# Kernel optimization log

Hardware: AMD Instinct MI355X
Metric: run time of the kernel (lower is better)

## Reference

```python
import jax, jax.numpy as jnp
import numpy as np

EMBED = 768
HEADS = 12
HEAD_DIM = EMBED // HEADS
RANK = 16
EPS = 1e-6
SCALE = 1.0 / np.sqrt(HEAD_DIM)


def setup_inputs() -> dict:
    key = jax.random.key(0)
    ks = jax.random.split(key, 12)
    B, S = 4, 1024
    hidden_states = jax.random.normal(ks[0], (B, S, EMBED), dtype=jnp.float32)
    attention_mask = jnp.zeros((B, 1, 1, S), dtype=jnp.float32)
    w = lambda k: jax.random.normal(k, (EMBED, EMBED), dtype=jnp.float32) * 0.02
    b = lambda k: jax.random.normal(k, (EMBED,), dtype=jnp.float32) * 0.02
    A = jax.random.normal(ks[9], (HEADS, HEAD_DIM, RANK), dtype=jnp.float32) * 0.05
    return {
        "hidden_states": hidden_states,
        "attention_mask": attention_mask,
        "Wq": w(ks[1]), "bq": b(ks[2]),
        "Wk": w(ks[3]), "bk": b(ks[4]),
        "Wv": w(ks[5]), "bv": b(ks[6]),
        "Wo": w(ks[7]), "bo": b(ks[8]),
        "A": A,
    }


def reference(hidden_states, attention_mask, Wq, bq, Wk, bk, Wv, bv, Wo, bo, A):
    B, S, E = hidden_states.shape
    H, D = HEADS, HEAD_DIM

    def proj(W, bias):
        y = hidden_states @ W.T + bias          # (B,S,E), torch Linear: x W^T + b
        return y.reshape(B, S, H, D).transpose(0, 2, 1, 3)  # (B,H,S,D)

    q = proj(Wq, bq)
    k = proj(Wk, bk)
    v = proj(Wv, bv)

    # Low-rank SPD Mahalanobis: G_h = A_h A_h^T + eps*I
    # d^2(x,y) = ||A^T(x-y)||^2 + eps*||x-y||^2 (block-diagonal per batch)
    qA = jnp.einsum("bhsd,hdr->bhsr", q, A)    # (B,H,S,R)
    kA = jnp.einsum("bhsd,hdr->bhsr", k, A)
    qq = jnp.sum(qA * qA, -1) + EPS * jnp.sum(q * q, -1)  # (B,H,S)
    kk = jnp.sum(kA * kA, -1) + EPS * jnp.sum(k * k, -1)
    cross = jnp.einsum("bhsr,bhtr->bhst", qA, kA) + EPS * jnp.einsum("bhsd,bhtd->bhst", q, k)
    d2 = qq[..., :, None] + kk[..., None, :] - 2.0 * cross  # (B,H,S,S)

    scores = -d2 * SCALE + attention_mask      # mask broadcasts (B,1,1,S)
    weights = jax.nn.softmax(scores, axis=-1)  # dropout p is identity in eval
    ctx = jnp.einsum("bhst,bhtd->bhsd", weights, v)
    ctx = ctx.transpose(0, 2, 1, 3).reshape(B, S, E)
    return ctx @ Wo.T + bo
```

## Files before the change

kernel.cpp:

```cpp
#include <hip/hip_runtime.h>

typedef __attribute__((ext_vector_type(8))) short s16x8;
typedef __attribute__((ext_vector_type(4))) float f32x4;
typedef __attribute__((ext_vector_type(4))) unsigned int u32x4;
typedef unsigned short u16;
typedef unsigned int u32;
typedef unsigned long long u64;

__device__ __forceinline__ u16 f2bf(float f) {
  u32 u = __float_as_uint(f);
  u32 r = u + 0x7fffu + ((u >> 16) & 1u);
  return (u16)(r >> 16);
}
__device__ __forceinline__ float bf2f(u16 h) {
  return __uint_as_float(((u32)h) << 16);
}

typedef __attribute__((address_space(3))) char lds_char_t;
typedef __attribute__((address_space(1))) const char glb_char_t;
__device__ __forceinline__ void gl2lds16(const void* g, void* l) {
  __builtin_amdgcn_global_load_lds((glb_char_t*)g, (lds_char_t*)l, 16, 0, 0);
}

#define HS_N 3145728
#define W_N  589824

__global__ __launch_bounds__(256) void convert_kernel(
    const float* __restrict__ hs, const float* __restrict__ wq, const float* __restrict__ wk,
    const float* __restrict__ wv, const float* __restrict__ wo,
    const float* __restrict__ bq, const float* __restrict__ bk, const float* __restrict__ bv,
    u16* __restrict__ hsb, u16* __restrict__ wqkvb, u16* __restrict__ wob,
    float* __restrict__ biasqkv)
{
  int t = blockIdx.x * 256 + threadIdx.x;
  long i = (long)t * 8;
  const float* src;
  u16* dst;
  if (i < HS_N)              { src = hs + i;                  dst = hsb + i; }
  else if (i < HS_N + W_N)   { src = wq + (i - HS_N);         dst = wqkvb + (i - HS_N); }
  else if (i < HS_N + 2*W_N) { src = wk + (i - HS_N - W_N);   dst = wqkvb + (i - HS_N); }
  else if (i < HS_N + 3*W_N) { src = wv + (i - HS_N - 2*W_N); dst = wqkvb + (i - HS_N); }
  else                       { src = wo + (i - HS_N - 3*W_N); dst = wob + (i - HS_N - 3*W_N); }
  float4 a = ((const float4*)src)[0];
  float4 b = ((const float4*)src)[1];
  uint4 o;
  o.x = (u32)f2bf(a.x) | ((u32)f2bf(a.y) << 16);
  o.y = (u32)f2bf(a.z) | ((u32)f2bf(a.w) << 16);
  o.z = (u32)f2bf(b.x) | ((u32)f2bf(b.y) << 16);
  o.w = (u32)f2bf(b.z) | ((u32)f2bf(b.w) << 16);
  *(uint4*)dst = o;
  if (t < 2304) biasqkv[t] = (t < 768) ? bq[t] : ((t < 1536) ? bk[t - 768] : bv[t - 1536]);
}

template<int MODE>
__global__ __launch_bounds__(256, 2) void gemm_bt(
    const u16* __restrict__ A, const u16* __restrict__ Bt, const float* __restrict__ bias,
    float* __restrict__ outF, u16* __restrict__ Qb, u16* __restrict__ Kb, u16* __restrict__ Vtb)
{
  constexpr int NT = (MODE == 0) ? 18 : 6;
  constexpr int CPX = NT * 64 / 8;

  __shared__ __align__(16) char sm[73728];
  char* const smA = sm;
  char* const smB = sm + 24576;

  const int tid = threadIdx.x;
  const int lane = tid & 63;
  const int w = tid >> 6;
  const int l15 = lane & 15, g = lane >> 4;
  const int wid = (blockIdx.x & 7) * CPX + (blockIdx.x >> 3);
  const int bx = wid % NT, by = wid / NT;
  const int mBase = by * 64;
  const int nBase = bx * 128;
  const int wr = w >> 1, wc = w & 1;
  const int mW = wr * 32, nW = wc * 64;

  f32x4 zero = {0.f, 0.f, 0.f, 0.f};
  f32x4 acc[2][4];
  #pragma unroll
  for (int i = 0; i < 2; i++)
    #pragma unroll
    for (int j = 0; j < 4; j++) acc[i][j] = zero;

  const u16* Arow = A + (long)mBase * 768;
  const u16* Brow = Bt + (long)nBase * 768;

  auto stage = [&](int c, int kb) {
    const int k0 = c * 64;
    #pragma unroll
    for (int i = 0; i < 2; i++) {
      int o = (i * 256 + tid) * 16;
      int r = o >> 7;
      int sl = ((o >> 4) & 7) ^ (r & 7);
      gl2lds16(Arow + (long)r * 768 + k0 + sl * 8,
               smA + kb * 8192 + i * 4096 + w * 1024);
    }
    #pragma unroll
    for (int i = 0; i < 4; i++) {
      int o = (i * 256 + tid) * 16;
      int r = o >> 7;
      int sl = ((o >> 4) & 7) ^ (r & 7);
      gl2lds16(Brow + (long)r * 768 + k0 + sl * 8,
               smB + kb * 16384 + i * 4096 + w * 1024);
    }
  };

  auto compute = [&](int kb) {
    const char* bufA = smA + kb * 8192;
    const char* bufB = smB + kb * 16384;
    #pragma unroll
    for (int kh = 0; kh < 2; kh++) {
      s16x8 af[2], bf[4];
      #pragma unroll
      for (int mi = 0; mi < 2; mi++) {
        int R = mW + mi * 16 + l15;
        af[mi] = *(const s16x8*)(bufA + R * 128 + (((kh * 4 + g) ^ (l15 & 7)) << 4));
      }
      #pragma unroll
      for (int ni = 0; ni < 4; ni++) {
        int R = nW + ni * 16 + l15;
        bf[ni] = *(const s16x8*)(bufB + R * 128 + (((kh * 4 + g) ^ (l15 & 7)) << 4));
      }
      #pragma unroll
      for (int mi = 0; mi < 2; mi++)
        #pragma unroll
        for (int ni = 0; ni < 4; ni++)
          acc[mi][ni] = __builtin_amdgcn_mfma_f32_16x16x32_bf16(af[mi], bf[ni], acc[mi][ni], 0, 0, 0);
    }
  };

  auto body = [&](int c, int kb, int kbn) {
    if (c < 11) { stage(c + 1, kbn); asm volatile("s_waitcnt vmcnt(6)" ::: "memory"); }
    else        { asm volatile("s_waitcnt vmcnt(0)" ::: "memory"); }
    asm volatile("s_barrier" ::: "memory");
    compute(kb);
  };

  stage(0, 0);
  #pragma unroll 1
  for (int cc = 0; cc < 4; cc++) {
    body(cc * 3,     0, 1);
    body(cc * 3 + 1, 1, 2);
    body(cc * 3 + 2, 2, 0);
  }
  __syncthreads();

  const int b_ = mBase >> 10;
  const int s0b = mBase & 1023;

  if constexpr (MODE == 1) {
    #pragma unroll
    for (int mi = 0; mi < 2; mi++)
      #pragma unroll
      for (int ni = 0; ni < 4; ni++) {
        int n = nBase + nW + ni * 16 + l15;
        int m0 = mBase + mW + mi * 16 + g * 4;
        float bb = bias[n];
        outF[(long)m0 * 768 + n]       = acc[mi][ni][0] + bb;
        outF[(long)(m0 + 1) * 768 + n] = acc[mi][ni][1] + bb;
        outF[(long)(m0 + 2) * 768 + n] = acc[mi][ni][2] + bb;
        outF[(long)(m0 + 3) * 768 + n] = acc[mi][ni][3] + bb;
      }
  } else {
    const int typ = bx / 6;
    if (typ < 2) {
      u16* qk = (typ == 0) ? Qb : Kb;
      #pragma unroll
      for (int mi = 0; mi < 2; mi++)
        #pragma unroll
        for (int ni = 0; ni < 4; ni++) {
          int n = nBase + nW + ni * 16 + l15;
          int hn = n - typ * 768;
          int h = hn >> 6, d = hn & 63;
          long bh = (long)b_ * 12 + h;
          int s0 = s0b + mW + mi * 16 + g * 4;
          float bb = bias[n];
          u16* dst = qk + (bh << 16) + ((long)s0 << 6) + d;
          dst[0]   = f2bf(acc[mi][ni][0] + bb);
          dst[64]  = f2bf(acc[mi][ni][1] + bb);
          dst[128] = f2bf(acc[mi][ni][2] + bb);
          dst[192] = f2bf(acc[mi][ni][3] + bb);
        }
    } else {
      u16* ct = (u16*)sm;
      #pragma unroll
      for (int mi = 0; mi < 2; mi++)
        #pragma unroll
        for (int ni = 0; ni < 4; ni++) {
          int nr = nW + ni * 16 + l15;
          int mr = mW + mi * 16 + g * 4;
          float bb = bias[nBase + nr];
          u32 lo = (u32)f2bf(acc[mi][ni][0] + bb) | ((u32)f2bf(acc[mi][ni][1] + bb) << 16);
          u32 hi = (u32)f2bf(acc[mi][ni][2] + bb) | ((u32)f2bf(acc[mi][ni][3] + bb) << 16);
          *(u64*)(ct + nr * 72 + mr) = (u64)lo | ((u64)hi << 32);
        }
      __syncthreads();
      int dr = tid >> 1, part = tid & 1;
      int hn = (bx - 12) * 128 + dr;
      int h = hn >> 6, d = hn & 63;
      long bh = (long)b_ * 12 + h;
      u16* dst = Vtb + (bh << 16) + (d << 10) + s0b + part * 32;
      const u16* srl = ct + dr * 72 + part * 32;
      #pragma unroll
      for (int i = 0; i < 4; i++)
        *(uint4*)(dst + i * 8) = *(const uint4*)(srl + i * 8);
    }
  }
}

__global__ __launch_bounds__(256) void qk_ext_kernel(
    const u16* __restrict__ Qb, const u16* __restrict__ Kb, const float* __restrict__ Am,
    const float* __restrict__ mask, u16* __restrict__ qAe, u16* __restrict__ kAe,
    float* __restrict__ beta2)
{
  const bool isK = blockIdx.x >= 192;
  const int rb = blockIdx.x * 256 - (isK ? 49152 : 0);
  const int h = (rb >> 10) % 12;
  const int row = rb + threadIdx.x;
  const int bh = row >> 10;
  const int s = row & 1023;
  const int b_ = bh / 12;

  const u16* src = (isK ? Kb : Qb) + ((long)row << 6);
  union { uint4 v4[8]; u32 u[32]; } c;
  #pragma unroll
  for (int i = 0; i < 8; i++) c.v4[i] = ((const uint4*)src)[i];

  const float* Ah = Am + h * 1024;
  float acc[16];
  #pragma unroll
  for (int r = 0; r < 16; r++) acc[r] = 0.f;
  float s2 = 0.f;
  #pragma unroll
  for (int d = 0; d < 64; d++) {
    u32 wd = c.u[d >> 1];
    float qd = bf2f((u16)((d & 1) ? (wd >> 16) : (wd & 0xffffu)));
    s2 += qd * qd;
    #pragma unroll
    for (int r = 0; r < 16; r++) acc[r] += qd * Ah[d * 16 + r];
  }

  union { u16 us[128]; uint4 v4[16]; } o;
  const float sA = isK ? 1.0f : 0.25f;
  const float sQ = isK ? 1e-3f : 0.25e-3f;
  #pragma unroll
  for (int r = 0; r < 16; r++) o.us[r] = f2bf(acc[r] * sA);
  #pragma unroll
  for (int d = 0; d < 64; d++) {
    u32 wd = c.u[d >> 1];
    float qd = bf2f((u16)((d & 1) ? (wd >> 16) : (wd & 0xffffu)));
    o.us[16 + d] = f2bf(qd * sQ);
  }
  #pragma unroll
  for (int j = 80; j < 128; j++) o.us[j] = 0;

  u16* dst = (isK ? kAe : qAe) + ((long)row << 7);
  #pragma unroll
  for (int i = 0; i < 16; i++) ((uint4*)dst)[i] = o.v4[i];

  if (isK) {
    float kk = 1e-6f * s2;
    #pragma unroll
    for (int r = 0; r < 16; r++) kk += acc[r] * acc[r];
    beta2[row] = -0.125f * kk + mask[(b_ << 10) + s];
  }
}

__global__ __launch_bounds__(128, 2) void attn_kernel(
    const u16* __restrict__ qAe, const u16* __restrict__ kAe, const u16* __restrict__ Vtb,
    const float* __restrict__ beta2, u16* __restrict__ ctxb)
{
  const int tid = threadIdx.x;
  const int lane = tid & 63;
  const int w = tid >> 6;
  const int l15 = lane & 15, g = lane >> 4;
  const int wid = (blockIdx.x & 7) * 96 + (blockIdx.x >> 3);
  const int bh = wid >> 4;
  const int qt = wid & 15;
  const int q0 = qt * 64 + w * 32;

  __shared__ __align__(16) char sm[2 * 8192 + 2 * 2560];
  char* kb0 = sm;
  char* kb1 = sm + 8192;
  char* Pw  = sm + 16384 + w * 2560;

  const u16* qbase = qAe + ((long)(bh * 1024 + q0) << 7);
  const u16* kbase = kAe + ((long)bh << 17);
  const u16* vbase = Vtb + ((long)bh << 16);
  const float* betab = beta2 + (bh << 10);

  u32x4 bqv[2][3];
  #pragma unroll
  for (int qf = 0; qf < 2; qf++)
    #pragma unroll
    for (int ks = 0; ks < 3; ks++) {
      const u16* a = qbase + ((qf * 16 + l15) << 7) + ks * 32 + g * 8;
      asm volatile("global_load_dwordx4 %0, %1, off" : "=v"(bqv[qf][ks]) : "v"(a));
    }

  auto stageK = [&](int c, char* buf) {
    const int t0 = c * 32;
    #pragma unroll
    for (int i2 = 0; i2 < 4; i2++) {
      int i = w * 4 + i2;
      int r = i * 4 + (lane >> 4);
      int col = ((lane & 15) ^ (r & 7)) * 8;
      const u16* gsrc = kbase + (long)(t0 + r) * 128 + col;
      gl2lds16(gsrc, buf + i * 1024);
    }
  };
  auto loadV = [&](int c, u32x4 (&dst)[4]) {
    const int t0 = c * 32;
    #pragma unroll
    for (int df = 0; df < 4; df++) {
      const u16* a = vbase + ((df * 16 + l15) << 10) + t0 + g * 8;
      asm volatile("global_load_dwordx4 %0, %1, off" : "=v"(dst[df]) : "v"(a));
    }
  };
  auto loadB = [&](int c, u32x4 (&dst)[2]) {
    #pragma unroll
    for (int tf = 0; tf < 2; tf++) {
      const float* a = betab + c * 32 + tf * 16 + g * 4;
      asm volatile("global_load_dwordx4 %0, %1, off" : "=v"(dst[tf]) : "v"(a));
    }
  };

  f32x4 zero = {0.f, 0.f, 0.f, 0.f};
  f32x4 cacc[2][4];
  #pragma unroll
  for (int a = 0; a < 2; a++)
    #pragma unroll
    for (int b = 0; b < 4; b++) cacc[a][b] = zero;
  float rsum[2] = {0.f, 0.f};

  u32x4 vA[4], vB[4], bA[2], bB[2];

  auto chunk = [&](auto LASTC, int c, char* bufc, char* bufn,
                   u32x4 (&curV)[4], u32x4 (&curB)[2],
                   u32x4 (&nxtV)[4], u32x4 (&nxtB)[2]) {
    constexpr bool LAST = decltype(LASTC)::value;
    asm volatile("s_waitcnt vmcnt(6)" ::: "memory");
    asm volatile("s_barrier" ::: "memory");
    if constexpr (!LAST) {
      stageK(c + 1, bufn);
      loadV(c + 1, nxtV);
      loadB(c + 1, nxtB);
    }
    f32x4 sacc[2][2];
    sacc[0][0] = zero; sacc[0][1] = zero; sacc[1][0] = zero; sacc[1][1] = zero;
    #pragma unroll
    for (int tf = 0; tf < 2; tf++)
      #pragma unroll
      for (int ks = 0; ks < 3; ks++) {
        s16x8 ak = *(const s16x8*)(bufc + (tf * 16 + l15) * 256 +
                                   ((ks * 64 + g * 16) ^ ((l15 & 7) << 4)));
        s16x8 b0 = __builtin_bit_cast(s16x8, bqv[0][ks]);
        s16x8 b1 = __builtin_bit_cast(s16x8, bqv[1][ks]);
        sacc[tf][0] = __builtin_amdgcn_mfma_f32_16x16x32_bf16(ak, b0, sacc[tf][0], 0, 0, 0);
        sacc[tf][1] = __builtin_amdgcn_mfma_f32_16x16x32_bf16(ak, b1, sacc[tf][1], 0, 0, 0);
      }
    if constexpr (!LAST) asm volatile("s_waitcnt vmcnt(10)" ::: "memory");
    else                 asm volatile("s_waitcnt vmcnt(0)" ::: "memory");
    __builtin_amdgcn_sched_barrier(0);
    #pragma unroll
    for (int tf = 0; tf < 2; tf++) {
      f32x4 bb = __builtin_bit_cast(f32x4, curB[tf]);
      #pragma unroll
      for (int qf = 0; qf < 2; qf++) {
        float e0 = __expf(sacc[tf][qf][0] + bb[0]);
        float e1 = __expf(sacc[tf][qf][1] + bb[1]);
        float e2 = __expf(sacc[tf][qf][2] + bb[2]);
        float e3 = __expf(sacc[tf][qf][3] + bb[3]);
        rsum[qf] += e0 + e1 + e2 + e3;
        u32 lo = (u32)f2bf(e0) | ((u32)f2bf(e1) << 16);
        u32 hi = (u32)f2bf(e2) | ((u32)f2bf(e3) << 16);
        *(u64*)(Pw + (qf * 16 + l15) * 80 + tf * 32 + g * 8) =
            (u64)lo | ((u64)hi << 32);
      }
    }
    #pragma unroll
    for (int qf = 0; qf < 2; qf++) {
      s16x8 ap = *(const s16x8*)(Pw + (qf * 16 + l15) * 80 + g * 16);
      #pragma unroll
      for (int df = 0; df < 4; df++) {
        s16x8 bv = __builtin_bit_cast(s16x8, curV[df]);
        cacc[qf][df] = __builtin_amdgcn_mfma_f32_16x16x32_bf16(ap, bv, cacc[qf][df], 0, 0, 0);
      }
    }
  };

  stageK(0, kb0);
  loadV(0, vA);
  loadB(0, bA);

  std::integral_constant<bool, false> F;
  std::integral_constant<bool, true>  T;
  #pragma unroll 1
  for (int c2 = 0; c2 < 15; c2++) {
    chunk(F, 2 * c2,     kb0, kb1, vA, bA, vB, bB);
    chunk(F, 2 * c2 + 1, kb1, kb0, vB, bB, vA, bA);
  }
  chunk(F, 30, kb0, kb1, vA, bA, vB, bB);
  chunk(T, 31, kb1, kb0, vB, bB, vA, bA);

  #pragma unroll
  for (int qf = 0; qf < 2; qf++) {
    rsum[qf] += __shfl_xor(rsum[qf], 16);
    rsum[qf] += __shfl_xor(rsum[qf], 32);
  }
  const int b_ = bh / 12, h = bh % 12;
  #pragma unroll
  for (int qf = 0; qf < 2; qf++) {
    #pragma unroll
    for (int j = 0; j < 4; j++) {
      float rs = __shfl(rsum[qf], g * 4 + j);
      float rinv = 1.0f / rs;
      int qg = q0 + qf * 16 + g * 4 + j;
      long base = ((long)(b_ * 1024 + qg)) * 768 + h * 64;
      #pragma unroll
      for (int df = 0; df < 4; df++)
        ctxb[base + df * 16 + l15] = f2bf(cacc[qf][df][j] * rinv);
    }
  }
}

extern "C" void kernel_launch(void* const* d_in, const int* in_sizes, int n_in,
                              void* d_out, int out_size, void* d_ws, size_t ws_size,
                              hipStream_t stream)
{
  (void)in_sizes; (void)n_in; (void)out_size; (void)ws_size;
  const float* hs   = (const float*)d_in[0];
  const float* mask = (const float*)d_in[1];
  const float* Wq   = (const float*)d_in[2];
  const float* bq   = (const float*)d_in[3];
  const float* Wk   = (const float*)d_in[4];
  const float* bk   = (const float*)d_in[5];
  const float* Wv   = (const float*)d_in[6];
  const float* bv   = (const float*)d_in[7];
  const float* Wo   = (const float*)d_in[8];
  const float* bo   = (const float*)d_in[9];
  const float* Am   = (const float*)d_in[10];
  float* out = (float*)d_out;

  char* p = (char*)d_ws;
  u16* hsb      = (u16*)p;   p += 6291456;
  u16* wqkvb    = (u16*)p;   p += 3538944;
  u16* wob      = (u16*)p;   p += 1179648;
  float* biasqkv= (float*)p; p += 9216;
  u16* Qb       = (u16*)p;   p += 6291456;
  u16* Kb       = (u16*)p;   p += 6291456;
  u16* Vtb      = (u16*)p;   p += 6291456;
  u16* qAeb     = (u16*)p;   p += 12582912;
  u16* kAeb     = (u16*)p;   p += 12582912;
  float* beta2  = (float*)p; p += 196608;
  u16* ctxb     = (u16*)p;   p += 6291456;

  convert_kernel<<<2688, 256, 0, stream>>>(hs, Wq, Wk, Wv, Wo, bq, bk, bv,
                                           hsb, wqkvb, wob, biasqkv);
  gemm_bt<0><<<1152, 256, 0, stream>>>(hsb, wqkvb, biasqkv,
                                       nullptr, Qb, Kb, Vtb);
  qk_ext_kernel<<<384, 256, 0, stream>>>(Qb, Kb, Am, mask, qAeb, kAeb, beta2);
  attn_kernel<<<768, 128, 0, stream>>>(qAeb, kAeb, Vtb, beta2, ctxb);
  gemm_bt<1><<<384, 256, 0, stream>>>(ctxb, wob, bo, out,
                                      nullptr, nullptr, nullptr);
}
```

Baseline: 98.41 us.

## Restructure attention to single-wave blocks with register-prefetched K and LDS bias

The attention kernel moves from 128-thread blocks that share K tiles through double-buffered LDS to 64-thread single-wave blocks. Each wave now loads K straight into registers with a double-buffered prefetch, so the barrier is gone. The whole bias row is staged into LDS once per block instead of loaded per chunk. Softmax is folded into base-2 by scaling q and beta by log2e upstream, so the kernel can use raw v_exp_f32 and packed bf16 conversion, with s_setprio raised around the MFMA sections. In exchange, K traffic is no longer shared across two waves and register pressure goes up.

```diff
diff --git a/kernel.cpp b/kernel.cpp
--- a/kernel.cpp
+++ b/kernel.cpp
@@ -3,6 +3,7 @@
 typedef __attribute__((ext_vector_type(8))) short s16x8;
 typedef __attribute__((ext_vector_type(4))) float f32x4;
 typedef __attribute__((ext_vector_type(4))) unsigned int u32x4;
+typedef __attribute__((ext_vector_type(2))) unsigned int u32x2;
 typedef unsigned short u16;
 typedef unsigned int u32;
 typedef unsigned long long u64;
@@ -24,6 +25,7 @@
 
 #define HS_N 3145728
 #define W_N  589824
+#define LOG2E 1.44269504f
 
 __global__ __launch_bounds__(256) void convert_kernel(
     const float* __restrict__ hs, const float* __restrict__ wq, const float* __restrict__ wk,
@@ -241,8 +243,8 @@
   }
 
   union { u16 us[128]; uint4 v4[16]; } o;
-  const float sA = isK ? 1.0f : 0.25f;
-  const float sQ = isK ? 1e-3f : 0.25e-3f;
+  const float sA = isK ? 1.0f : 0.25f * LOG2E;
+  const float sQ = isK ? 1e-3f : 0.25e-3f * LOG2E;
   #pragma unroll
   for (int r = 0; r < 16; r++) o.us[r] = f2bf(acc[r] * sA);
   #pragma unroll
@@ -262,27 +264,22 @@
     float kk = 1e-6f * s2;
     #pragma unroll
     for (int r = 0; r < 16; r++) kk += acc[r] * acc[r];
-    beta2[row] = -0.125f * kk + mask[(b_ << 10) + s];
-  }
-}
-
-__global__ __launch_bounds__(128, 2) void attn_kernel(
+    beta2[row] = LOG2E * (-0.125f * kk + mask[(b_ << 10) + s]);
+  }
+}
+
+__global__ __launch_bounds__(64, 2) void attn_kernel(
     const u16* __restrict__ qAe, const u16* __restrict__ kAe, const u16* __restrict__ Vtb,
     const float* __restrict__ beta2, u16* __restrict__ ctxb)
 {
-  const int tid = threadIdx.x;
-  const int lane = tid & 63;
-  const int w = tid >> 6;
+  const int lane = threadIdx.x & 63;
   const int l15 = lane & 15, g = lane >> 4;
-  const int wid = (blockIdx.x & 7) * 96 + (blockIdx.x >> 3);
-  const int bh = wid >> 4;
-  const int qt = wid & 15;
-  const int q0 = qt * 64 + w * 32;
-
-  __shared__ __align__(16) char sm[2 * 8192 + 2 * 2560];
-  char* kb0 = sm;
-  char* kb1 = sm + 8192;
-  char* Pw  = sm + 16384 + w * 2560;
+  const int wid = ((int)blockIdx.x & 7) * 192 + ((int)blockIdx.x >> 3);
+  const int bh = wid >> 5;
+  const int q0 = (wid & 31) * 32;
+
+  __shared__ __align__(16) char Pw[32 * 80];
+  __shared__ __align__(16) float Blds[1024];
 
   const u16* qbase = qAe + ((long)(bh * 1024 + q0) << 7);
   const u16* kbase = kAe + ((long)bh << 17);
@@ -297,17 +294,19 @@
       const u16* a = qbase + ((qf * 16 + l15) << 7) + ks * 32 + g * 8;
       asm volatile("global_load_dwordx4 %0, %1, off" : "=v"(bqv[qf][ks]) : "v"(a));
     }
-
-  auto stageK = [&](int c, char* buf) {
-    const int t0 = c * 32;
-    #pragma unroll
-    for (int i2 = 0; i2 < 4; i2++) {
-      int i = w * 4 + i2;
-      int r = i * 4 + (lane >> 4);
-      int col = ((lane & 15) ^ (r & 7)) * 8;
-      const u16* gsrc = kbase + (long)(t0 + r) * 128 + col;
-      gl2lds16(gsrc, buf + i * 1024);
-    }
+  #pragma unroll
+  for (int i = 0; i < 4; i++)
+    gl2lds16(betab + i * 256 + lane * 4, (char*)Blds + i * 1024);
+
+  auto loadK = [&](int c, u32x4 (&dst)[6]) {
+    const long t0 = (long)c * 32;
+    #pragma unroll
+    for (int tf = 0; tf < 2; tf++)
+      #pragma unroll
+      for (int ks = 0; ks < 3; ks++) {
+        const u16* a = kbase + (t0 + tf * 16 + l15) * 128 + ks * 32 + g * 8;
+        asm volatile("global_load_dwordx4 %0, %1, off" : "=v"(dst[tf * 3 + ks]) : "v"(a));
+      }
   };
   auto loadV = [&](int c, u32x4 (&dst)[4]) {
     const int t0 = c * 32;
@@ -317,13 +316,6 @@
       asm volatile("global_load_dwordx4 %0, %1, off" : "=v"(dst[df]) : "v"(a));
     }
   };
-  auto loadB = [&](int c, u32x4 (&dst)[2]) {
-    #pragma unroll
-    for (int tf = 0; tf < 2; tf++) {
-      const float* a = betab + c * 32 + tf * 16 + g * 4;
-      asm volatile("global_load_dwordx4 %0, %1, off" : "=v"(dst[tf]) : "v"(a));
-    }
-  };
 
   f32x4 zero = {0.f, 0.f, 0.f, 0.f};
   f32x4 cacc[2][4];
@@ -333,51 +325,60 @@
     for (int b = 0; b < 4; b++) cacc[a][b] = zero;
   float rsum[2] = {0.f, 0.f};
 
-  u32x4 vA[4], vB[4], bA[2], bB[2];
-
-  auto chunk = [&](auto LASTC, int c, char* bufc, char* bufn,
-                   u32x4 (&curV)[4], u32x4 (&curB)[2],
-                   u32x4 (&nxtV)[4], u32x4 (&nxtB)[2]) {
+  u32x4 kA[6], kB[6], vA[4], vB[4];
+
+  auto chunk = [&](auto LASTC, int c,
+                   u32x4 (&curK)[6], u32x4 (&curV)[4],
+                   u32x4 (&nxtK)[6], u32x4 (&nxtV)[4]) {
     constexpr bool LAST = decltype(LASTC)::value;
-    asm volatile("s_waitcnt vmcnt(6)" ::: "memory");
-    asm volatile("s_barrier" ::: "memory");
     if constexpr (!LAST) {
-      stageK(c + 1, bufn);
+      loadK(c + 1, nxtK);
       loadV(c + 1, nxtV);
-      loadB(c + 1, nxtB);
-    }
+      asm volatile("s_waitcnt vmcnt(14)" ::: "memory");
+    } else {
+      asm volatile("s_waitcnt vmcnt(4)" ::: "memory");
+    }
+    __builtin_amdgcn_sched_barrier(0);
+
+    __builtin_amdgcn_s_setprio(1);
     f32x4 sacc[2][2];
     sacc[0][0] = zero; sacc[0][1] = zero; sacc[1][0] = zero; sacc[1][1] = zero;
     #pragma unroll
     for (int tf = 0; tf < 2; tf++)
       #pragma unroll
       for (int ks = 0; ks < 3; ks++) {
-        s16x8 ak = *(const s16x8*)(bufc + (tf * 16 + l15) * 256 +
-                                   ((ks * 64 + g * 16) ^ ((l15 & 7) << 4)));
+        s16x8 ak = __builtin_bit_cast(s16x8, curK[tf * 3 + ks]);
         s16x8 b0 = __builtin_bit_cast(s16x8, bqv[0][ks]);
         s16x8 b1 = __builtin_bit_cast(s16x8, bqv[1][ks]);
         sacc[tf][0] = __builtin_amdgcn_mfma_f32_16x16x32_bf16(ak, b0, sacc[tf][0], 0, 0, 0);
         sacc[tf][1] = __builtin_amdgcn_mfma_f32_16x16x32_bf16(ak, b1, sacc[tf][1], 0, 0, 0);
       }
+    __builtin_amdgcn_s_setprio(0);
+
     if constexpr (!LAST) asm volatile("s_waitcnt vmcnt(10)" ::: "memory");
     else                 asm volatile("s_waitcnt vmcnt(0)" ::: "memory");
     __builtin_amdgcn_sched_barrier(0);
+
     #pragma unroll
     for (int tf = 0; tf < 2; tf++) {
-      f32x4 bb = __builtin_bit_cast(f32x4, curB[tf]);
+      f32x4 bb = *(const f32x4*)((const char*)Blds + c * 128 + tf * 64 + g * 16);
       #pragma unroll
       for (int qf = 0; qf < 2; qf++) {
-        float e0 = __expf(sacc[tf][qf][0] + bb[0]);
-        float e1 = __expf(sacc[tf][qf][1] + bb[1]);
-        float e2 = __expf(sacc[tf][qf][2] + bb[2]);
-        float e3 = __expf(sacc[tf][qf][3] + bb[3]);
-        rsum[qf] += e0 + e1 + e2 + e3;
-        u32 lo = (u32)f2bf(e0) | ((u32)f2bf(e1) << 16);
-        u32 hi = (u32)f2bf(e2) | ((u32)f2bf(e3) << 16);
-        *(u64*)(Pw + (qf * 16 + l15) * 80 + tf * 32 + g * 8) =
-            (u64)lo | ((u64)hi << 32);
-      }
-    }
+        float e0, e1, e2, e3;
+        asm("v_exp_f32 %0, %1" : "=v"(e0) : "v"(sacc[tf][qf][0] + bb[0]));
+        asm("v_exp_f32 %0, %1" : "=v"(e1) : "v"(sacc[tf][qf][1] + bb[1]));
+        asm("v_exp_f32 %0, %1" : "=v"(e2) : "v"(sacc[tf][qf][2] + bb[2]));
+        asm("v_exp_f32 %0, %1" : "=v"(e3) : "v"(sacc[tf][qf][3] + bb[3]));
+        rsum[qf] += (e0 + e1) + (e2 + e3);
+        u32 p01, p23;
+        asm("v_cvt_pk_bf16_f32 %0, %1, %2" : "=v"(p01) : "v"(e0), "v"(e1));
+        asm("v_cvt_pk_bf16_f32 %0, %1, %2" : "=v"(p23) : "v"(e2), "v"(e3));
+        u32x2 pk = {p01, p23};
+        *(u32x2*)(Pw + (qf * 16 + l15) * 80 + tf * 32 + g * 8) = pk;
+      }
+    }
+
+    __builtin_amdgcn_s_setprio(1);
     #pragma unroll
     for (int qf = 0; qf < 2; qf++) {
       s16x8 ap = *(const s16x8*)(Pw + (qf * 16 + l15) * 80 + g * 16);
@@ -387,21 +388,21 @@
         cacc[qf][df] = __builtin_amdgcn_mfma_f32_16x16x32_bf16(ap, bv, cacc[qf][df], 0, 0, 0);
       }
     }
-  };
-
-  stageK(0, kb0);
+    __builtin_amdgcn_s_setprio(0);
+  };
+
+  loadK(0, kA);
   loadV(0, vA);
-  loadB(0, bA);
 
   std::integral_constant<bool, false> F;
   std::integral_constant<bool, true>  T;
   #pragma unroll 1
   for (int c2 = 0; c2 < 15; c2++) {
-    chunk(F, 2 * c2,     kb0, kb1, vA, bA, vB, bB);
-    chunk(F, 2 * c2 + 1, kb1, kb0, vB, bB, vA, bA);
-  }
-  chunk(F, 30, kb0, kb1, vA, bA, vB, bB);
-  chunk(T, 31, kb1, kb0, vB, bB, vA, bA);
+    chunk(F, 2 * c2,     kA, vA, kB, vB);
+    chunk(F, 2 * c2 + 1, kB, vB, kA, vA);
+  }
+  chunk(F, 30, kA, vA, kB, vB);
+  chunk(T, 31, kB, vB, kA, vA);
 
   #pragma unroll
   for (int qf = 0; qf < 2; qf++) {
@@ -460,7 +461,7 @@
   gemm_bt<0><<<1152, 256, 0, stream>>>(hsb, wqkvb, biasqkv,
                                        nullptr, Qb, Kb, Vtb);
   qk_ext_kernel<<<384, 256, 0, stream>>>(Qb, Kb, Am, mask, qAeb, kAeb, beta2);
-  attn_kernel<<<768, 128, 0, stream>>>(qAeb, kAeb, Vtb, beta2, ctxb);
+  attn_kernel<<<1536, 64, 0, stream>>>(qAeb, kAeb, Vtb, beta2, ctxb);
   gemm_bt<1><<<384, 256, 0, stream>>>(ctxb, wob, bo, out,
                                       nullptr, nullptr, nullptr);
 }
```

Result: slower. 120.5 us (+22.4%).

## Split attention work across four waves per block and use native exp2

Applied to the files above, without the earlier changes.

The attention kernel now launches 256 threads per block, with four waves each owning 16 query rows instead of two waves owning 32. This halves per-wave accumulator and Q-register state, which targets higher occupancy and more latency hiding. K staging is split across four waves, so the same K/V tile traffic is shared by more waves. The log2(e) factor is folded into the q-side scales and beta so softmax can use raw v_exp_f32 and packed bf16 conversion, cutting ALU work in the exp path. The cost is that each wave now loads V and beta separately, which doubles per-block global V/beta traffic per query.

```diff
diff --git a/kernel.cpp b/kernel.cpp
--- a/kernel.cpp
+++ b/kernel.cpp
@@ -3,6 +3,7 @@
 typedef __attribute__((ext_vector_type(8))) short s16x8;
 typedef __attribute__((ext_vector_type(4))) float f32x4;
 typedef __attribute__((ext_vector_type(4))) unsigned int u32x4;
+typedef __attribute__((ext_vector_type(2))) unsigned int u32x2;
 typedef unsigned short u16;
 typedef unsigned int u32;
 typedef unsigned long long u64;
@@ -24,6 +25,7 @@
 
 #define HS_N 3145728
 #define W_N  589824
+#define LOG2E 1.44269504f
 
 __global__ __launch_bounds__(256) void convert_kernel(
     const float* __restrict__ hs, const float* __restrict__ wq, const float* __restrict__ wk,
@@ -241,8 +243,8 @@
   }
 
   union { u16 us[128]; uint4 v4[16]; } o;
-  const float sA = isK ? 1.0f : 0.25f;
-  const float sQ = isK ? 1e-3f : 0.25e-3f;
+  const float sA = isK ? 1.0f : 0.25f * LOG2E;
+  const float sQ = isK ? 1e-3f : 0.25e-3f * LOG2E;
   #pragma unroll
   for (int r = 0; r < 16; r++) o.us[r] = f2bf(acc[r] * sA);
   #pragma unroll
@@ -262,11 +264,11 @@
     float kk = 1e-6f * s2;
     #pragma unroll
     for (int r = 0; r < 16; r++) kk += acc[r] * acc[r];
-    beta2[row] = -0.125f * kk + mask[(b_ << 10) + s];
-  }
-}
-
-__global__ __launch_bounds__(128, 2) void attn_kernel(
+    beta2[row] = LOG2E * (-0.125f * kk + mask[(b_ << 10) + s]);
+  }
+}
+
+__global__ __launch_bounds__(256, 3) void attn_kernel(
     const u16* __restrict__ qAe, const u16* __restrict__ kAe, const u16* __restrict__ Vtb,
     const float* __restrict__ beta2, u16* __restrict__ ctxb)
 {
@@ -274,39 +276,36 @@
   const int lane = tid & 63;
   const int w = tid >> 6;
   const int l15 = lane & 15, g = lane >> 4;
-  const int wid = (blockIdx.x & 7) * 96 + (blockIdx.x >> 3);
+  const int wid = ((int)blockIdx.x & 7) * 96 + ((int)blockIdx.x >> 3);
   const int bh = wid >> 4;
   const int qt = wid & 15;
-  const int q0 = qt * 64 + w * 32;
-
-  __shared__ __align__(16) char sm[2 * 8192 + 2 * 2560];
-  char* kb0 = sm;
-  char* kb1 = sm + 8192;
-  char* Pw  = sm + 16384 + w * 2560;
+  const int q0 = qt * 64 + w * 16;
+
+  __shared__ __align__(16) char sm[16384 + 4 * 1280];
+  char* const kb0 = sm;
+  char* const kb1 = sm + 8192;
+  char* const Pw  = sm + 16384 + w * 1280;
 
   const u16* qbase = qAe + ((long)(bh * 1024 + q0) << 7);
   const u16* kbase = kAe + ((long)bh << 17);
   const u16* vbase = Vtb + ((long)bh << 16);
   const float* betab = beta2 + (bh << 10);
 
-  u32x4 bqv[2][3];
-  #pragma unroll
-  for (int qf = 0; qf < 2; qf++)
-    #pragma unroll
-    for (int ks = 0; ks < 3; ks++) {
-      const u16* a = qbase + ((qf * 16 + l15) << 7) + ks * 32 + g * 8;
-      asm volatile("global_load_dwordx4 %0, %1, off" : "=v"(bqv[qf][ks]) : "v"(a));
-    }
+  u32x4 bqv[3];
+  #pragma unroll
+  for (int ks = 0; ks < 3; ks++) {
+    const u16* a = qbase + (l15 << 7) + ks * 32 + g * 8;
+    asm volatile("global_load_dwordx4 %0, %1, off" : "=v"(bqv[ks]) : "v"(a));
+  }
 
   auto stageK = [&](int c, char* buf) {
     const int t0 = c * 32;
     #pragma unroll
-    for (int i2 = 0; i2 < 4; i2++) {
-      int i = w * 4 + i2;
+    for (int i2 = 0; i2 < 2; i2++) {
+      int i = w * 2 + i2;
       int r = i * 4 + (lane >> 4);
       int col = ((lane & 15) ^ (r & 7)) * 8;
-      const u16* gsrc = kbase + (long)(t0 + r) * 128 + col;
-      gl2lds16(gsrc, buf + i * 1024);
+      gl2lds16(kbase + (long)(t0 + r) * 128 + col, buf + i * 1024);
     }
   };
   auto loadV = [&](int c, u32x4 (&dst)[4]) {
@@ -326,12 +325,10 @@
   };
 
   f32x4 zero = {0.f, 0.f, 0.f, 0.f};
-  f32x4 cacc[2][4];
-  #pragma unroll
-  for (int a = 0; a < 2; a++)
-    #pragma unroll
-    for (int b = 0; b < 4; b++) cacc[a][b] = zero;
-  float rsum[2] = {0.f, 0.f};
+  f32x4 cacc[4];
+  #pragma unroll
+  for (int b = 0; b < 4; b++) cacc[b] = zero;
+  float rsum = 0.f;
 
   u32x4 vA[4], vB[4], bA[2], bB[2];
 
@@ -343,53 +340,49 @@
     asm volatile("s_barrier" ::: "memory");
     if constexpr (!LAST) {
       stageK(c + 1, bufn);
+      __builtin_amdgcn_sched_barrier(0);
       loadV(c + 1, nxtV);
       loadB(c + 1, nxtB);
     }
-    f32x4 sacc[2][2];
-    sacc[0][0] = zero; sacc[0][1] = zero; sacc[1][0] = zero; sacc[1][1] = zero;
+    f32x4 sacc[2];
+    sacc[0] = zero; sacc[1] = zero;
     #pragma unroll
     for (int tf = 0; tf < 2; tf++)
       #pragma unroll
       for (int ks = 0; ks < 3; ks++) {
         s16x8 ak = *(const s16x8*)(bufc + (tf * 16 + l15) * 256 +
                                    ((ks * 64 + g * 16) ^ ((l15 & 7) << 4)));
-        s16x8 b0 = __builtin_bit_cast(s16x8, bqv[0][ks]);
-        s16x8 b1 = __builtin_bit_cast(s16x8, bqv[1][ks]);
-        sacc[tf][0] = __builtin_amdgcn_mfma_f32_16x16x32_bf16(ak, b0, sacc[tf][0], 0, 0, 0);
-        sacc[tf][1] = __builtin_amdgcn_mfma_f32_16x16x32_bf16(ak, b1, sacc[tf][1], 0, 0, 0);
+        s16x8 bq = __builtin_bit_cast(s16x8, bqv[ks]);
+        sacc[tf] = __builtin_amdgcn_mfma_f32_16x16x32_bf16(ak, bq, sacc[tf], 0, 0, 0);
       }
-    if constexpr (!LAST) asm volatile("s_waitcnt vmcnt(10)" ::: "memory");
+    if constexpr (!LAST) asm volatile("s_waitcnt vmcnt(8)" ::: "memory");
     else                 asm volatile("s_waitcnt vmcnt(0)" ::: "memory");
     __builtin_amdgcn_sched_barrier(0);
     #pragma unroll
     for (int tf = 0; tf < 2; tf++) {
       f32x4 bb = __builtin_bit_cast(f32x4, curB[tf]);
-      #pragma unroll
-      for (int qf = 0; qf < 2; qf++) {
-        float e0 = __expf(sacc[tf][qf][0] + bb[0]);
-        float e1 = __expf(sacc[tf][qf][1] + bb[1]);
-        float e2 = __expf(sacc[tf][qf][2] + bb[2]);
-        float e3 = __expf(sacc[tf][qf][3] + bb[3]);
-        rsum[qf] += e0 + e1 + e2 + e3;
-        u32 lo = (u32)f2bf(e0) | ((u32)f2bf(e1) << 16);
-        u32 hi = (u32)f2bf(e2) | ((u32)f2bf(e3) << 16);
-        *(u64*)(Pw + (qf * 16 + l15) * 80 + tf * 32 + g * 8) =
-            (u64)lo | ((u64)hi << 32);
-      }
-    }
-    #pragma unroll
-    for (int qf = 0; qf < 2; qf++) {
-      s16x8 ap = *(const s16x8*)(Pw + (qf * 16 + l15) * 80 + g * 16);
-      #pragma unroll
-      for (int df = 0; df < 4; df++) {
-        s16x8 bv = __builtin_bit_cast(s16x8, curV[df]);
-        cacc[qf][df] = __builtin_amdgcn_mfma_f32_16x16x32_bf16(ap, bv, cacc[qf][df], 0, 0, 0);
-      }
+      float e0, e1, e2, e3;
+      asm("v_exp_f32 %0, %1" : "=v"(e0) : "v"(sacc[tf][0] + bb[0]));
+      asm("v_exp_f32 %0, %1" : "=v"(e1) : "v"(sacc[tf][1] + bb[1]));
+      asm("v_exp_f32 %0, %1" : "=v"(e2) : "v"(sacc[tf][2] + bb[2]));
+      asm("v_exp_f32 %0, %1" : "=v"(e3) : "v"(sacc[tf][3] + bb[3]));
+      rsum += (e0 + e1) + (e2 + e3);
+      u32 p01, p23;
+      asm("v_cvt_pk_bf16_f32 %0, %1, %2" : "=v"(p01) : "v"(e0), "v"(e1));
+      asm("v_cvt_pk_bf16_f32 %0, %1, %2" : "=v"(p23) : "v"(e2), "v"(e3));
+      u32x2 pk = {p01, p23};
+      *(u32x2*)(Pw + l15 * 80 + tf * 32 + g * 8) = pk;
+    }
+    s16x8 ap = *(const s16x8*)(Pw + l15 * 80 + g * 16);
+    #pragma unroll
+    for (int df = 0; df < 4; df++) {
+      s16x8 bv = __builtin_bit_cast(s16x8, curV[df]);
+      cacc[df] = __builtin_amdgcn_mfma_f32_16x16x32_bf16(ap, bv, cacc[df], 0, 0, 0);
     }
   };
 
   stageK(0, kb0);
+  __builtin_amdgcn_sched_barrier(0);
   loadV(0, vA);
   loadB(0, bA);
 
@@ -403,24 +396,18 @@
   chunk(F, 30, kb0, kb1, vA, bA, vB, bB);
   chunk(T, 31, kb1, kb0, vB, bB, vA, bA);
 
-  #pragma unroll
-  for (int qf = 0; qf < 2; qf++) {
-    rsum[qf] += __shfl_xor(rsum[qf], 16);
-    rsum[qf] += __shfl_xor(rsum[qf], 32);
-  }
+  rsum += __shfl_xor(rsum, 16);
+  rsum += __shfl_xor(rsum, 32);
   const int b_ = bh / 12, h = bh % 12;
   #pragma unroll
-  for (int qf = 0; qf < 2; qf++) {
-    #pragma unroll
-    for (int j = 0; j < 4; j++) {
-      float rs = __shfl(rsum[qf], g * 4 + j);
-      float rinv = 1.0f / rs;
-      int qg = q0 + qf * 16 + g * 4 + j;
-      long base = ((long)(b_ * 1024 + qg)) * 768 + h * 64;
-      #pragma unroll
-      for (int df = 0; df < 4; df++)
-        ctxb[base + df * 16 + l15] = f2bf(cacc[qf][df][j] * rinv);
-    }
+  for (int j = 0; j < 4; j++) {
+    float rs = __shfl(rsum, g * 4 + j);
+    float rinv = 1.0f / rs;
+    int qg = q0 + g * 4 + j;
+    long base = ((long)(b_ * 1024 + qg)) * 768 + h * 64;
+    #pragma unroll
+    for (int df = 0; df < 4; df++)
+      ctxb[base + df * 16 + l15] = f2bf(cacc[df][j] * rinv);
   }
 }
 
@@ -460,7 +447,7 @@
   gemm_bt<0><<<1152, 256, 0, stream>>>(hsb, wqkvb, biasqkv,
                                        nullptr, Qb, Kb, Vtb);
   qk_ext_kernel<<<384, 256, 0, stream>>>(Qb, Kb, Am, mask, qAeb, kAeb, beta2);
-  attn_kernel<<<768, 128, 0, stream>>>(qAeb, kAeb, Vtb, beta2, ctxb);
+  attn_kernel<<<768, 256, 0, stream>>>(qAeb, kAeb, Vtb, beta2, ctxb);
   gemm_bt<1><<<384, 256, 0, stream>>>(ctxb, wob, bo, out,
                                       nullptr, nullptr, nullptr);
 }
```

Result: slower. 118.8 us (+20.7%).

## Software-pipeline attention with triple-buffered K and QK of next chunk overlapping softmax

Applied to the files above, without the earlier changes.

Restructures the attention loop so the QK^T MFMAs for chunk c+1 run while the exp and PV of chunk c proceed. K is staged two chunks ahead into a third LDS buffer, which removes the barrier stall between staging and compute. It also folds log2(e) into the precomputed Q scale and beta so the kernel can use raw v_exp_f32, and uses the hardware v_cvt_pk_bf16_f32 for packing. The cost is more LDS and registers (two score accumulator sets), which may reduce occupancy.

```diff
diff --git a/kernel.cpp b/kernel.cpp
--- a/kernel.cpp
+++ b/kernel.cpp
@@ -3,6 +3,7 @@
 typedef __attribute__((ext_vector_type(8))) short s16x8;
 typedef __attribute__((ext_vector_type(4))) float f32x4;
 typedef __attribute__((ext_vector_type(4))) unsigned int u32x4;
+typedef __attribute__((ext_vector_type(2))) unsigned int u32x2;
 typedef unsigned short u16;
 typedef unsigned int u32;
 typedef unsigned long long u64;
@@ -24,6 +25,7 @@
 
 #define HS_N 3145728
 #define W_N  589824
+#define LOG2E 1.44269504f
 
 __global__ __launch_bounds__(256) void convert_kernel(
     const float* __restrict__ hs, const float* __restrict__ wq, const float* __restrict__ wk,
@@ -241,8 +243,8 @@
   }
 
   union { u16 us[128]; uint4 v4[16]; } o;
-  const float sA = isK ? 1.0f : 0.25f;
-  const float sQ = isK ? 1e-3f : 0.25e-3f;
+  const float sA = isK ? 1.0f : 0.25f * LOG2E;
+  const float sQ = isK ? 1e-3f : 0.25e-3f * LOG2E;
   #pragma unroll
   for (int r = 0; r < 16; r++) o.us[r] = f2bf(acc[r] * sA);
   #pragma unroll
@@ -262,7 +264,7 @@
     float kk = 1e-6f * s2;
     #pragma unroll
     for (int r = 0; r < 16; r++) kk += acc[r] * acc[r];
-    beta2[row] = -0.125f * kk + mask[(b_ << 10) + s];
+    beta2[row] = LOG2E * (-0.125f * kk + mask[(b_ << 10) + s]);
   }
 }
 
@@ -274,15 +276,16 @@
   const int lane = tid & 63;
   const int w = tid >> 6;
   const int l15 = lane & 15, g = lane >> 4;
-  const int wid = (blockIdx.x & 7) * 96 + (blockIdx.x >> 3);
+  const int wid = ((int)blockIdx.x & 7) * 96 + ((int)blockIdx.x >> 3);
   const int bh = wid >> 4;
   const int qt = wid & 15;
   const int q0 = qt * 64 + w * 32;
 
-  __shared__ __align__(16) char sm[2 * 8192 + 2 * 2560];
-  char* kb0 = sm;
-  char* kb1 = sm + 8192;
-  char* Pw  = sm + 16384 + w * 2560;
+  __shared__ __align__(16) char sm[3 * 8192 + 2 * 2560];
+  char* const kb0 = sm;
+  char* const kb1 = sm + 8192;
+  char* const kb2 = sm + 16384;
+  char* const Pw  = sm + 24576 + w * 2560;
 
   const u16* qbase = qAe + ((long)(bh * 1024 + q0) << 7);
   const u16* kbase = kAe + ((long)bh << 17);
@@ -305,8 +308,7 @@
       int i = w * 4 + i2;
       int r = i * 4 + (lane >> 4);
       int col = ((lane & 15) ^ (r & 7)) * 8;
-      const u16* gsrc = kbase + (long)(t0 + r) * 128 + col;
-      gl2lds16(gsrc, buf + i * 1024);
+      gl2lds16(kbase + (long)(t0 + r) * 128 + col, buf + i * 1024);
     }
   };
   auto loadV = [&](int c, u32x4 (&dst)[4]) {
@@ -334,74 +336,98 @@
   float rsum[2] = {0.f, 0.f};
 
   u32x4 vA[4], vB[4], bA[2], bB[2];
-
-  auto chunk = [&](auto LASTC, int c, char* bufc, char* bufn,
-                   u32x4 (&curV)[4], u32x4 (&curB)[2],
-                   u32x4 (&nxtV)[4], u32x4 (&nxtB)[2]) {
-    constexpr bool LAST = decltype(LASTC)::value;
-    asm volatile("s_waitcnt vmcnt(6)" ::: "memory");
-    asm volatile("s_barrier" ::: "memory");
-    if constexpr (!LAST) {
-      stageK(c + 1, bufn);
-      loadV(c + 1, nxtV);
-      loadB(c + 1, nxtB);
-    }
-    f32x4 sacc[2][2];
-    sacc[0][0] = zero; sacc[0][1] = zero; sacc[1][0] = zero; sacc[1][1] = zero;
+  f32x4 sA[2][2], sB[2][2];
+
+  auto qk = [&](const char* kbuf, f32x4 (&s)[2][2]) {
+    s[0][0] = zero; s[0][1] = zero; s[1][0] = zero; s[1][1] = zero;
     #pragma unroll
     for (int tf = 0; tf < 2; tf++)
       #pragma unroll
       for (int ks = 0; ks < 3; ks++) {
-        s16x8 ak = *(const s16x8*)(bufc + (tf * 16 + l15) * 256 +
+        s16x8 ak = *(const s16x8*)(kbuf + (tf * 16 + l15) * 256 +
                                    ((ks * 64 + g * 16) ^ ((l15 & 7) << 4)));
         s16x8 b0 = __builtin_bit_cast(s16x8, bqv[0][ks]);
         s16x8 b1 = __builtin_bit_cast(s16x8, bqv[1][ks]);
-        sacc[tf][0] = __builtin_amdgcn_mfma_f32_16x16x32_bf16(ak, b0, sacc[tf][0], 0, 0, 0);
-        sacc[tf][1] = __builtin_amdgcn_mfma_f32_16x16x32_bf16(ak, b1, sacc[tf][1], 0, 0, 0);
-      }
-    if constexpr (!LAST) asm volatile("s_waitcnt vmcnt(10)" ::: "memory");
-    else                 asm volatile("s_waitcnt vmcnt(0)" ::: "memory");
+        s[tf][0] = __builtin_amdgcn_mfma_f32_16x16x32_bf16(ak, b0, s[tf][0], 0, 0, 0);
+        s[tf][1] = __builtin_amdgcn_mfma_f32_16x16x32_bf16(ak, b1, s[tf][1], 0, 0, 0);
+      }
+  };
+
+  auto iter = [&](auto VNC, auto STGC, auto QKC, int c, char* sbuf, const char* kbuf,
+                  u32x4 (&vcur)[4], u32x4 (&bcur)[2],
+                  u32x4 (&vnxt)[4], u32x4 (&bnxt)[2],
+                  f32x4 (&scur)[2][2], f32x4 (&snxt)[2][2]) {
+    constexpr int  VN    = decltype(VNC)::value;
+    constexpr bool DOSTG = decltype(STGC)::value;
+    constexpr bool DOQK  = decltype(QKC)::value;
+    if constexpr (DOSTG) {
+      stageK(c + 2, sbuf);
+      __builtin_amdgcn_sched_barrier(0);
+    }
+    if constexpr (DOQK) { loadV(c + 1, vnxt); loadB(c + 1, bnxt); }
+    if constexpr (VN == 10)     asm volatile("s_waitcnt vmcnt(10)" ::: "memory");
+    else if constexpr (VN == 6) asm volatile("s_waitcnt vmcnt(6)"  ::: "memory");
+    else                        asm volatile("s_waitcnt vmcnt(0)"  ::: "memory");
+    asm volatile("s_barrier" ::: "memory");
     __builtin_amdgcn_sched_barrier(0);
     #pragma unroll
     for (int tf = 0; tf < 2; tf++) {
-      f32x4 bb = __builtin_bit_cast(f32x4, curB[tf]);
+      f32x4 bb = __builtin_bit_cast(f32x4, bcur[tf]);
       #pragma unroll
       for (int qf = 0; qf < 2; qf++) {
-        float e0 = __expf(sacc[tf][qf][0] + bb[0]);
-        float e1 = __expf(sacc[tf][qf][1] + bb[1]);
-        float e2 = __expf(sacc[tf][qf][2] + bb[2]);
-        float e3 = __expf(sacc[tf][qf][3] + bb[3]);
-        rsum[qf] += e0 + e1 + e2 + e3;
-        u32 lo = (u32)f2bf(e0) | ((u32)f2bf(e1) << 16);
-        u32 hi = (u32)f2bf(e2) | ((u32)f2bf(e3) << 16);
-        *(u64*)(Pw + (qf * 16 + l15) * 80 + tf * 32 + g * 8) =
-            (u64)lo | ((u64)hi << 32);
-      }
-    }
+        float e0, e1, e2, e3;
+        asm("v_exp_f32 %0, %1" : "=v"(e0) : "v"(scur[tf][qf][0] + bb[0]));
+        asm("v_exp_f32 %0, %1" : "=v"(e1) : "v"(scur[tf][qf][1] + bb[1]));
+        asm("v_exp_f32 %0, %1" : "=v"(e2) : "v"(scur[tf][qf][2] + bb[2]));
+        asm("v_exp_f32 %0, %1" : "=v"(e3) : "v"(scur[tf][qf][3] + bb[3]));
+        rsum[qf] += (e0 + e1) + (e2 + e3);
+        u32 p01, p23;
+        asm("v_cvt_pk_bf16_f32 %0, %1, %2" : "=v"(p01) : "v"(e0), "v"(e1));
+        asm("v_cvt_pk_bf16_f32 %0, %1, %2" : "=v"(p23) : "v"(e2), "v"(e3));
+        u32x2 pk = {p01, p23};
+        *(u32x2*)(Pw + (qf * 16 + l15) * 80 + tf * 32 + g * 8) = pk;
+      }
+    }
+    if constexpr (DOQK) qk(kbuf, snxt);
     #pragma unroll
     for (int qf = 0; qf < 2; qf++) {
       s16x8 ap = *(const s16x8*)(Pw + (qf * 16 + l15) * 80 + g * 16);
       #pragma unroll
       for (int df = 0; df < 4; df++) {
-        s16x8 bv = __builtin_bit_cast(s16x8, curV[df]);
+        s16x8 bv = __builtin_bit_cast(s16x8, vcur[df]);
         cacc[qf][df] = __builtin_amdgcn_mfma_f32_16x16x32_bf16(ap, bv, cacc[qf][df], 0, 0, 0);
       }
     }
   };
 
   stageK(0, kb0);
+  stageK(1, kb1);
+  __builtin_amdgcn_sched_barrier(0);
   loadV(0, vA);
   loadB(0, bA);
-
-  std::integral_constant<bool, false> F;
-  std::integral_constant<bool, true>  T;
+  asm volatile("s_waitcnt vmcnt(10)" ::: "memory");
+  asm volatile("s_barrier" ::: "memory");
+  __builtin_amdgcn_sched_barrier(0);
+  qk(kb0, sA);
+
+  std::integral_constant<int, 10> V10;
+  std::integral_constant<int, 6>  V6;
+  std::integral_constant<int, 0>  V0;
+  std::integral_constant<bool, true>  Tt;
+  std::integral_constant<bool, false> Ff;
+
   #pragma unroll 1
-  for (int c2 = 0; c2 < 15; c2++) {
-    chunk(F, 2 * c2,     kb0, kb1, vA, bA, vB, bB);
-    chunk(F, 2 * c2 + 1, kb1, kb0, vB, bB, vA, bA);
-  }
-  chunk(F, 30, kb0, kb1, vA, bA, vB, bB);
-  chunk(T, 31, kb1, kb0, vB, bB, vA, bA);
+  for (int c6 = 0; c6 < 5; c6++) {
+    int c = c6 * 6;
+    iter(V10, Tt, Tt, c + 0, kb2, kb1, vA, bA, vB, bB, sA, sB);
+    iter(V10, Tt, Tt, c + 1, kb0, kb2, vB, bB, vA, bA, sB, sA);
+    iter(V10, Tt, Tt, c + 2, kb1, kb0, vA, bA, vB, bB, sA, sB);
+    iter(V10, Tt, Tt, c + 3, kb2, kb1, vB, bB, vA, bA, sB, sA);
+    iter(V10, Tt, Tt, c + 4, kb0, kb2, vA, bA, vB, bB, sA, sB);
+    iter(V10, Tt, Tt, c + 5, kb1, kb0, vB, bB, vA, bA, sB, sA);
+  }
+  iter(V6, Ff, Tt, 30, kb0, kb1, vA, bA, vB, bB, sA, sB);
+  iter(V0, Ff, Ff, 31, kb0, kb0, vB, bB, vA, bA, sB, sA);
 
   #pragma unroll
   for (int qf = 0; qf < 2; qf++) {
```

Measured after the change: 111.7 us. 13.5% more time.
